# Performance work log

Hardware: AMD Instinct MI355X
Metric: run time of the kernel (lower is better)

The kernel has to match this reference:

```python
import jax, jax.numpy as jnp
import numpy as np

T = 16384
G = 8
D_IN = 2048
D_OUT = 8192
# uneven per-expert group sizes summing exactly to T (torch.split requires this)
_GROUP_SIZES = np.array([1024, 3072, 2048, 512, 4096, 1536, 2560, 1536], dtype=np.int64)
assert _GROUP_SIZES.sum() == T


def setup_inputs() -> dict:
    key = jax.random.key(0)
    k_x, k_w = jax.random.split(key)
    hidden_states = jax.random.normal(k_x, (T, D_IN), dtype=jnp.float32)
    # kaiming_uniform_(a=sqrt(5)) on [G, out, in] -> bound = 1/sqrt(in_features)
    bound = 1.0 / np.sqrt(D_IN)
    weight = jax.random.uniform(k_w, (G, D_OUT, D_IN), dtype=jnp.float32,
                                minval=-bound, maxval=bound)
    offsets = jnp.asarray(np.cumsum(_GROUP_SIZES), dtype=jnp.int64)
    return {"hidden_states": hidden_states, "offsets": offsets, "weight": weight}


def reference(hidden_states, offsets, weight):
    # grouped GEMM: for group g, rows [offsets[g-1]:offsets[g]] @ weight[g].T
    # weight is [G, out, in]; torch transposes last two dims -> rhs [G, in, out]
    group_sizes = jnp.diff(offsets, prepend=jnp.zeros((1,), offsets.dtype)).astype(jnp.int32)
    rhs = jnp.swapaxes(weight, -1, -2)  # [G, in, out]
    return jax.lax.ragged_dot(hidden_states, rhs, group_sizes)  # [T, out]
```

## Files before the change

kernel.cpp:

```cpp
#include <hip/hip_runtime.h>
#include <stdint.h>

#define T_TOK   16384
#define D_INK   2048
#define D_OUTN  8192
#define G_NUM   8

#define BM 256
#define BN 256
#define BK 64
#define NKT (D_INK / BK)
#define MT_TILES (T_TOK / BM)
#define NT_TILES (D_OUTN / BN)
#define MCHUNK 4

typedef __attribute__((ext_vector_type(8))) short bf16x8;
typedef __attribute__((ext_vector_type(4))) float f32x4;

#define BARRIER() do { asm volatile("" ::: "memory"); __builtin_amdgcn_s_barrier(); asm volatile("" ::: "memory"); } while (0)
#define VMCNT(n)  asm volatile("s_waitcnt vmcnt(" #n ")" ::: "memory")
#define MFMA16(d,va,vb) d = __builtin_amdgcn_mfma_f32_16x16x32_bf16(va, vb, d, 0, 0, 0)

__device__ __forceinline__ unsigned int f2bf(float f) {
    union { float f; unsigned int u; } v; v.f = f;
    unsigned int u = v.u;
    unsigned int r = u + 0x7FFFu + ((u >> 16) & 1u);
    return r >> 16;
}

__global__ __launch_bounds__(256) void cvt_f32_bf16(const float* __restrict__ src,
                                                    unsigned short* __restrict__ dst,
                                                    long long n8) {
    long long i = (long long)blockIdx.x * blockDim.x + threadIdx.x;
    long long stride = (long long)gridDim.x * blockDim.x;
    const float4* s4 = reinterpret_cast<const float4*>(src);
    for (; i < n8; i += stride) {
        float4 x = s4[i * 2];
        float4 y = s4[i * 2 + 1];
        uint4 o;
        o.x = f2bf(x.x) | (f2bf(x.y) << 16);
        o.y = f2bf(x.z) | (f2bf(x.w) << 16);
        o.z = f2bf(y.x) | (f2bf(y.y) << 16);
        o.w = f2bf(y.z) | (f2bf(y.w) << 16);
        *reinterpret_cast<uint4*>(dst + i * 8) = o;
    }
}

__device__ __forceinline__ void gload_lds16(const unsigned short* g, void* l) {
    __builtin_amdgcn_global_load_lds(
        (const __attribute__((address_space(1))) void*)g,
        (__attribute__((address_space(3))) void*)l,
        16, 0, 0);
}

__global__ __launch_bounds__(512, 2) void grouped_gemm_256(
    const unsigned short* __restrict__ Abf,
    const unsigned short* __restrict__ Wbf,
    const int* __restrict__ offs_raw,
    float* __restrict__ out)
{
    __shared__ unsigned short lds[2][32768];

    const int tid  = threadIdx.x;
    const int wave = tid >> 6;
    const int lane = tid & 63;

    const int swz = (blockIdx.x & 7) * (MT_TILES * NT_TILES / 8) + (blockIdx.x >> 3);
    const int per_chunk = MCHUNK * NT_TILES;
    const int chunk = swz / per_chunk;
    const int rem   = swz % per_chunk;
    const int nt = rem >> 2;
    const int mt = chunk * MCHUNK + (rem & (MCHUNK - 1));

    const int row0 = mt * BM;
    const int col0 = nt * BN;

    const int ostride = (offs_raw[1] == 0) ? 2 : 1;
    int g = 0;
#pragma unroll
    for (int i = 0; i < G_NUM - 1; ++i)
        if (row0 >= offs_raw[i * ostride]) g = i + 1;

    const unsigned short* Aorig = Abf + (size_t)row0 * D_INK;
    const unsigned short* Worig = Wbf + ((size_t)g * D_OUTN + col0) * D_INK;

    const int lrow = lane >> 2;
    const int gcol_off = ((lane & 3) * 8) ^ ((lane & 32) ? 16 : 0);

    const int fr  = lane & 15;
    const int fk2 = (lane >> 4) << 4;
    const int swz_off = fr * 64 + (fk2 ^ ((fr & 8) ? 32 : 0));
    const int wm16 = (wave >> 2) * 8;
    const int wn16 = (wave & 3) * 4;
    const int wm = (wave >> 2) * 128;
    const int wn = (wave & 3) * 64;

    char* ldsc = (char*)&lds[0][0];

    auto stageAh = [&](int buf, int kt, int h) {
#pragma unroll
        for (int i = 0; i < 2; ++i) {
            const int s = h * 16 + i * 8 + wave;
            const int sr = s >> 1, sc = s & 1;
            const unsigned short* src = Aorig + (size_t)(sr * 16 + lrow) * D_INK
                                        + kt * BK + sc * 32 + gcol_off;
            gload_lds16(src, ldsc + buf * 65536 + s * 1024);
        }
    };
    auto stageBh = [&](int buf, int kt, int h) {
#pragma unroll
        for (int i = 0; i < 2; ++i) {
            const int s = h * 16 + i * 8 + wave;
            const int sr = s >> 1, sc = s & 1;
            const unsigned short* src = Worig + (size_t)(sr * 16 + lrow) * D_INK
                                        + kt * BK + sc * 32 + gcol_off;
            gload_lds16(src, ldsc + buf * 65536 + 32768 + s * 1024);
        }
    };

    f32x4 acc[8][4] = {};
    bf16x8 a[4][2], b[4][2];

    auto ldB2 = [&](int buf, int jb) {
#pragma unroll
        for (int j = 0; j < 2; ++j) {
            const int sr = wn16 + jb + j;
            b[jb + j][0] = *reinterpret_cast<const bf16x8*>(ldsc + buf * 65536 + 32768 + (sr * 2 + 0) * 1024 + swz_off);
            b[jb + j][1] = *reinterpret_cast<const bf16x8*>(ldsc + buf * 65536 + 32768 + (sr * 2 + 1) * 1024 + swz_off);
        }
    };
    auto ldA4 = [&](int buf, int mb) {
#pragma unroll
        for (int i = 0; i < 4; ++i) {
            const int sr = wm16 + mb + i;
            a[i][0] = *reinterpret_cast<const bf16x8*>(ldsc + buf * 65536 + (sr * 2 + 0) * 1024 + swz_off);
            a[i][1] = *reinterpret_cast<const bf16x8*>(ldsc + buf * 65536 + (sr * 2 + 1) * 1024 + swz_off);
        }
    };
    auto quad = [&](int ib, int jb) {
        __builtin_amdgcn_s_setprio(1);
#pragma unroll
        for (int i = 0; i < 4; ++i)
#pragma unroll
            for (int j = 0; j < 2; ++j) {
                MFMA16(acc[ib + i][jb + j], a[i][0], b[jb + j][0]);
                MFMA16(acc[ib + i][jb + j], a[i][1], b[jb + j][1]);
            }
        __builtin_amdgcn_s_setprio(0);
    };

    stageBh(0, 0, 0); stageBh(0, 0, 1);
    stageAh(0, 0, 0); stageAh(0, 0, 1);
    stageBh(1, 1, 0); stageBh(1, 1, 1);
    VMCNT(4);
    BARRIER();

    for (int t = 0; t < NKT; t += 2) {
        const bool s2 = (t + 2 < NKT), s3 = (t + 3 < NKT);

        ldB2(0, 0); ldA4(0, 0);
        stageAh(1, t + 1, 0);
        BARRIER(); quad(0, 0); BARRIER();

        ldB2(0, 2);
        stageAh(1, t + 1, 1);
        BARRIER(); quad(0, 2); BARRIER();

        ldA4(0, 4);
        if (s2) stageBh(0, t + 2, 0);
        BARRIER(); quad(4, 0); BARRIER();

        if (s2) stageBh(0, t + 2, 1);
        BARRIER();
        quad(4, 2);
        if (s2) { VMCNT(4); } else { VMCNT(0); }
        BARRIER();

        ldB2(1, 0); ldA4(1, 0);
        if (s2) stageAh(0, t + 2, 0);
        BARRIER(); quad(0, 0); BARRIER();

        ldB2(1, 2);
        if (s2) stageAh(0, t + 2, 1);
        BARRIER(); quad(0, 2); BARRIER();

        ldA4(1, 4);
        if (s3) stageBh(1, t + 3, 0);
        BARRIER(); quad(4, 0); BARRIER();

        if (s3) stageBh(1, t + 3, 1);
        BARRIER();
        quad(4, 2);
        if (s3) { VMCNT(4); } else { VMCNT(0); }
        BARRIER();
    }

    const int crb = (lane >> 4) * 4;
#pragma unroll
    for (int i = 0; i < 8; ++i)
#pragma unroll
        for (int j = 0; j < 4; ++j)
#pragma unroll
            for (int r = 0; r < 4; ++r) {
                const int rr = row0 + wm + i * 16 + crb + r;
                const int cc = col0 + wn + j * 16 + fr;
                out[(size_t)rr * D_OUTN + cc] = acc[i][j][r];
            }
}

__global__ __launch_bounds__(256) void naive_grouped(
    const float* __restrict__ A, const float* __restrict__ W,
    const int* __restrict__ offs_raw, float* __restrict__ out)
{
    const long long total = (long long)T_TOK * D_OUTN;
    long long idx = (long long)blockIdx.x * blockDim.x + threadIdx.x;
    const long long stride = (long long)gridDim.x * blockDim.x;
    const int ostride = (offs_raw[1] == 0) ? 2 : 1;
    for (; idx < total; idx += stride) {
        const int t = (int)(idx / D_OUTN);
        const int c = (int)(idx % D_OUTN);
        int g = 0;
        for (int i = 0; i < G_NUM - 1; ++i)
            if (t >= offs_raw[i * ostride]) g = i + 1;
        const float4* a4 = reinterpret_cast<const float4*>(A + (size_t)t * D_INK);
        const float4* w4 = reinterpret_cast<const float4*>(W + ((size_t)g * D_OUTN + c) * D_INK);
        float s = 0.f;
        for (int k = 0; k < D_INK / 4; ++k) {
            float4 av = a4[k], wv = w4[k];
            s += av.x * wv.x + av.y * wv.y + av.z * wv.z + av.w * wv.w;
        }
        out[idx] = s;
    }
}

extern "C" void kernel_launch(void* const* d_in, const int* in_sizes, int n_in,
                              void* d_out, int out_size, void* d_ws, size_t ws_size,
                              hipStream_t stream) {
    const float* hidden = (const float*)d_in[0];
    const int*   offs   = (const int*)d_in[1];
    const float* weight = (const float*)d_in[2];
    float* out = (float*)d_out;

    const size_t nA = (size_t)T_TOK * D_INK;
    const size_t nW = (size_t)G_NUM * D_OUTN * D_INK;
    const size_t need = (nA + nW) * sizeof(unsigned short);

    if (ws_size >= need) {
        unsigned short* Abf = (unsigned short*)d_ws;
        unsigned short* Wbf = Abf + nA;
        cvt_f32_bf16<<<2048, 256, 0, stream>>>(hidden, Abf, (long long)(nA / 8));
        cvt_f32_bf16<<<4096, 256, 0, stream>>>(weight, Wbf, (long long)(nW / 8));
        grouped_gemm_256<<<MT_TILES * NT_TILES, 512, 0, stream>>>(Abf, Wbf, offs, out);
    } else {
        naive_grouped<<<8192, 256, 0, stream>>>(hidden, weight, offs, out);
    }
}
```

Baseline: 708.0 us.

## Swap MFMA operands for vectorized stores and prefetch next B fragment earlier

```diff
diff --git a/kernel.cpp b/kernel.cpp
--- a/kernel.cpp
+++ b/kernel.cpp
@@ -19,7 +19,7 @@
 
 #define BARRIER() do { asm volatile("" ::: "memory"); __builtin_amdgcn_s_barrier(); asm volatile("" ::: "memory"); } while (0)
 #define VMCNT(n)  asm volatile("s_waitcnt vmcnt(" #n ")" ::: "memory")
-#define MFMA16(d,va,vb) d = __builtin_amdgcn_mfma_f32_16x16x32_bf16(va, vb, d, 0, 0, 0)
+#define MFMA16(d,vw,vx) d = __builtin_amdgcn_mfma_f32_16x16x32_bf16(vw, vx, d, 0, 0, 0)
 
 __device__ __forceinline__ unsigned int f2bf(float f) {
     union { float f; unsigned int u; } v; v.f = f;
@@ -143,8 +143,8 @@
         for (int i = 0; i < 4; ++i)
 #pragma unroll
             for (int j = 0; j < 2; ++j) {
-                MFMA16(acc[ib + i][jb + j], a[i][0], b[jb + j][0]);
-                MFMA16(acc[ib + i][jb + j], a[i][1], b[jb + j][1]);
+                MFMA16(acc[ib + i][jb + j], b[jb + j][0], a[i][0]);
+                MFMA16(acc[ib + i][jb + j], b[jb + j][1], a[i][1]);
             }
         __builtin_amdgcn_s_setprio(0);
     };
@@ -154,58 +154,60 @@
     stageBh(1, 1, 0); stageBh(1, 1, 1);
     VMCNT(4);
     BARRIER();
+    ldB2(0, 0);
 
     for (int t = 0; t < NKT; t += 2) {
-        const bool s2 = (t + 2 < NKT), s3 = (t + 3 < NKT);
-
-        ldB2(0, 0); ldA4(0, 0);
+        const bool s2 = (t + 2 < NKT);
+
+        ldA4(0, 0); ldB2(0, 2);
         stageAh(1, t + 1, 0);
         BARRIER(); quad(0, 0); BARRIER();
 
-        ldB2(0, 2);
         stageAh(1, t + 1, 1);
         BARRIER(); quad(0, 2); BARRIER();
 
         ldA4(0, 4);
         if (s2) stageBh(0, t + 2, 0);
-        BARRIER(); quad(4, 0); BARRIER();
-
+        BARRIER(); quad(4, 0);
+        if (s2) { VMCNT(6); } else { VMCNT(0); }
+        BARRIER();
+
+        ldB2(1, 0);
         if (s2) stageBh(0, t + 2, 1);
-        BARRIER();
-        quad(4, 2);
+        BARRIER(); quad(4, 2);
         if (s2) { VMCNT(4); } else { VMCNT(0); }
         BARRIER();
 
-        ldB2(1, 0); ldA4(1, 0);
+        ldA4(1, 0); ldB2(1, 2);
         if (s2) stageAh(0, t + 2, 0);
         BARRIER(); quad(0, 0); BARRIER();
 
-        ldB2(1, 2);
         if (s2) stageAh(0, t + 2, 1);
         BARRIER(); quad(0, 2); BARRIER();
 
         ldA4(1, 4);
-        if (s3) stageBh(1, t + 3, 0);
-        BARRIER(); quad(4, 0); BARRIER();
-
-        if (s3) stageBh(1, t + 3, 1);
-        BARRIER();
-        quad(4, 2);
-        if (s3) { VMCNT(4); } else { VMCNT(0); }
-        BARRIER();
-    }
-
-    const int crb = (lane >> 4) * 4;
-#pragma unroll
-    for (int i = 0; i < 8; ++i)
-#pragma unroll
-        for (int j = 0; j < 4; ++j)
-#pragma unroll
-            for (int r = 0; r < 4; ++r) {
-                const int rr = row0 + wm + i * 16 + crb + r;
-                const int cc = col0 + wn + j * 16 + fr;
-                out[(size_t)rr * D_OUTN + cc] = acc[i][j][r];
-            }
+        if (s2) stageBh(1, t + 3, 0);
+        BARRIER(); quad(4, 0);
+        if (s2) { VMCNT(6); } else { VMCNT(0); }
+        BARRIER();
+
+        if (s2) { ldB2(0, 0); stageBh(1, t + 3, 1); }
+        BARRIER(); quad(4, 2);
+        if (s2) { VMCNT(4); } else { VMCNT(0); }
+        BARRIER();
+    }
+
+    const int m_in   = lane & 15;
+    const int n_base = (lane >> 4) * 4;
+#pragma unroll
+    for (int i = 0; i < 8; ++i) {
+        const size_t rbase = (size_t)(row0 + wm + i * 16 + m_in) * D_OUTN;
+#pragma unroll
+        for (int j = 0; j < 4; ++j) {
+            const int cc = col0 + wn + j * 16 + n_base;
+            *reinterpret_cast<f32x4*>(&out[rbase + cc]) = acc[i][j];
+        }
+    }
 }
 
 __global__ __launch_bounds__(256) void naive_grouped(
```

Measured after the change: 861.1 us. 21.6% more time.

## Swap MFMA operands for vectorized row stores and retile block swizzle

Applied to the files above, without the earlier changes.

```diff
diff --git a/kernel.cpp b/kernel.cpp
--- a/kernel.cpp
+++ b/kernel.cpp
@@ -12,14 +12,13 @@
 #define NKT (D_INK / BK)
 #define MT_TILES (T_TOK / BM)
 #define NT_TILES (D_OUTN / BN)
-#define MCHUNK 4
 
 typedef __attribute__((ext_vector_type(8))) short bf16x8;
 typedef __attribute__((ext_vector_type(4))) float f32x4;
 
 #define BARRIER() do { asm volatile("" ::: "memory"); __builtin_amdgcn_s_barrier(); asm volatile("" ::: "memory"); } while (0)
 #define VMCNT(n)  asm volatile("s_waitcnt vmcnt(" #n ")" ::: "memory")
-#define MFMA16(d,va,vb) d = __builtin_amdgcn_mfma_f32_16x16x32_bf16(va, vb, d, 0, 0, 0)
+#define MFMA16(d,vw,vx) d = __builtin_amdgcn_mfma_f32_16x16x32_bf16(vw, vx, d, 0, 0, 0)
 
 __device__ __forceinline__ unsigned int f2bf(float f) {
     union { float f; unsigned int u; } v; v.f = f;
@@ -66,11 +65,10 @@
     const int lane = tid & 63;
 
     const int swz = (blockIdx.x & 7) * (MT_TILES * NT_TILES / 8) + (blockIdx.x >> 3);
-    const int per_chunk = MCHUNK * NT_TILES;
-    const int chunk = swz / per_chunk;
-    const int rem   = swz % per_chunk;
-    const int nt = rem >> 2;
-    const int mt = chunk * MCHUNK + (rem & (MCHUNK - 1));
+    const int set = swz >> 5;
+    const int idx = swz & 31;
+    const int nt = (set & 7) * 4 + (idx & 3);
+    const int mt = (set >> 3) * 8 + (idx >> 2);
 
     const int row0 = mt * BM;
     const int col0 = nt * BN;
@@ -143,8 +141,8 @@
         for (int i = 0; i < 4; ++i)
 #pragma unroll
             for (int j = 0; j < 2; ++j) {
-                MFMA16(acc[ib + i][jb + j], a[i][0], b[jb + j][0]);
-                MFMA16(acc[ib + i][jb + j], a[i][1], b[jb + j][1]);
+                MFMA16(acc[ib + i][jb + j], b[jb + j][0], a[i][0]);
+                MFMA16(acc[ib + i][jb + j], b[jb + j][1], a[i][1]);
             }
         __builtin_amdgcn_s_setprio(0);
     };
@@ -195,17 +193,17 @@
         BARRIER();
     }
 
-    const int crb = (lane >> 4) * 4;
-#pragma unroll
-    for (int i = 0; i < 8; ++i)
-#pragma unroll
-        for (int j = 0; j < 4; ++j)
-#pragma unroll
-            for (int r = 0; r < 4; ++r) {
-                const int rr = row0 + wm + i * 16 + crb + r;
-                const int cc = col0 + wn + j * 16 + fr;
-                out[(size_t)rr * D_OUTN + cc] = acc[i][j][r];
-            }
+    const int m_in   = lane & 15;
+    const int n_base = (lane >> 4) * 4;
+#pragma unroll
+    for (int i = 0; i < 8; ++i) {
+        const size_t rbase = (size_t)(row0 + wm + i * 16 + m_in) * D_OUTN;
+#pragma unroll
+        for (int j = 0; j < 4; ++j) {
+            const int cc = col0 + wn + j * 16 + n_base;
+            *reinterpret_cast<f32x4*>(&out[rbase + cc]) = acc[i][j];
+        }
+    }
 }
 
 __global__ __launch_bounds__(256) void naive_grouped(
```

Result: slower. 724.5 us (+2.3%).
